# Kernel optimization log

Measured on AMD Instinct MI355X. Metric: run time of the kernel, lower is better.

Reference implementation:

```python
import jax, jax.numpy as jnp
import numpy as np

DIM = 1024
NUM_HEADS = 16
HEAD_DIM = DIM // NUM_HEADS
MLP_RATIO = 4
NUM_EXPERTS = 4
B, N = 4, 1024


def _ln(x, g, b, eps=1e-5):
    m = jnp.mean(x, axis=-1, keepdims=True)
    v = jnp.mean(jnp.square(x - m), axis=-1, keepdims=True)
    return (x - m) * jax.lax.rsqrt(v + eps) * g + b


def setup_inputs() -> dict:
    key = jax.random.key(0)
    ks = jax.random.split(key, 8)
    d = DIM
    return {
        "x": jax.random.normal(ks[0], (B, N, d), jnp.float32),
        "expert_mask": jax.random.randint(ks[1], (B, N), 0, NUM_EXPERTS),
        "expert_probs": jax.random.uniform(ks[2], (B, N, 1), jnp.float32),
        "expand_weight": 0.02 * jax.random.normal(ks[3], (3 * d + MLP_RATIO * d, d), jnp.float32),
        "mlp_bias": 0.02 * jax.random.normal(ks[4], (MLP_RATIO * d,), jnp.float32),
        "contract_weight": 0.02 * jax.random.normal(ks[5], (2 * d, d + MLP_RATIO * d), jnp.float32),
        "contract_bias": 0.02 * jax.random.normal(ks[6], (2 * d,), jnp.float32),
        "norm1_g": jnp.ones((d,), jnp.float32),
        "norm1_b": jnp.zeros((d,), jnp.float32),
        "norm2_g": jnp.ones((d,), jnp.float32),
        "norm2_b": jnp.zeros((d,), jnp.float32),
        "alpha": 0.1 * jax.random.normal(ks[7], (1,), jnp.float32),
    }


def reference(x, expert_mask, expert_probs, expand_weight, mlp_bias, contract_weight,
              contract_bias, norm1_g, norm1_b, norm2_g, norm2_b, alpha):
    Bx, Nx, D = x.shape
    # nested capacity per token: D_e = D // 2**(E-1-e)
    d_e = D // jnp.power(2, NUM_EXPERTS - 1 - expert_mask)          # [B,N] int
    fmask = (jnp.arange(D) < d_e[..., None]).astype(x.dtype)        # [B,N,D]

    residual = x
    # bias as in source: concat([mlp_bias, zeros(3d)]) added to full expand output
    input_bias = jnp.concatenate([mlp_bias, jnp.zeros((3 * D,), x.dtype)], axis=-1)

    # nested_linear_expand: token uses only first D_e input features
    xn = _ln(x, norm1_g, norm1_b) * fmask
    y = jnp.einsum('bnd,ed->bne', xn, expand_weight) + input_bias   # [B,N,7D]

    qkv = y[..., : 3 * D]
    mlp_hidden = y[..., 3 * D:] + mlp_bias                          # [B,N,4D]

    q = qkv[..., :D]
    k = _ln(qkv[..., D:2 * D], norm2_g, norm2_b)
    v = _ln(qkv[..., 2 * D:], norm2_g, norm2_b)

    def heads(t):
        return t.reshape(Bx, Nx, NUM_HEADS, HEAD_DIM).transpose(0, 2, 1, 3)

    scale = HEAD_DIM ** -0.5
    attn = jax.nn.softmax(jnp.einsum('bhqd,bhkd->bhqk', heads(q) * scale, heads(k)), axis=-1)
    attn_out = jnp.einsum('bhqk,bhkd->bhqd', attn, heads(v)).transpose(0, 2, 1, 3).reshape(Bx, Nx, D)

    h = jnp.concatenate([attn_out, jax.nn.gelu(mlp_hidden, approximate=False)], axis=-1)  # [B,N,5D]
    # nested_linear_contract: only first D_e outputs per D-sized half are produced
    out = jnp.einsum('bnf,of->bno', h, contract_weight) + contract_bias                   # [B,N,2D]
    out = out * jnp.concatenate([fmask, fmask], axis=-1)

    attn_branch = out[..., :D] + residual
    return attn_branch + (alpha * expert_probs + 1.0) * out[..., D:]
```

## Files before the change

kernel.cpp:

```cpp
#include <hip/hip_runtime.h>
#include <hip/hip_bf16.h>

typedef __attribute__((ext_vector_type(8))) short bf16x8;
typedef __attribute__((ext_vector_type(4))) short s16x4;
typedef __attribute__((ext_vector_type(4))) float f32x4;

#define DIM    1024
#define TOKENS 4096
#define NHEAD  16
#define HD     64
#define EXP_N  7168
#define CON_N  2048
#define HF     5120

#define WEXP_OFF 0u
#define XN_OFF   14680064u
#define WC_OFF   0u
#define Q_OFF    23068672u
#define K_OFF    31457280u
#define V_OFF    39845888u
#define H_OFF    48234496u
#define PERM_OFF 90177536u
#define DSRT_OFF 90193920u
#define TMAX_OFF 90210304u
#define OUT2_OFF 23068672u

__device__ __forceinline__ short f2bf(float f) {
  union { __hip_bfloat16 h; short s; } u;
  u.h = __float2bfloat16(f);
  return u.s;
}
__device__ __forceinline__ float bf2f(short s) {
  unsigned int u = ((unsigned int)(unsigned short)s) << 16;
  return __builtin_bit_cast(float, u);
}

__device__ __forceinline__ void gload16(const void* g, void* l) {
  __builtin_amdgcn_global_load_lds((const __attribute__((address_space(1))) void*)g,
                                   (__attribute__((address_space(3))) void*)l,
                                   16, 0, 0);
}

__device__ __forceinline__ void block_reduce_2(float& a, float& b) {
  #pragma unroll
  for (int off = 32; off > 0; off >>= 1) {
    a += __shfl_down(a, off);
    b += __shfl_down(b, off);
  }
  __shared__ float red[2][4];
  int wid = threadIdx.x >> 6, lane = threadIdx.x & 63;
  if (lane == 0) { red[0][wid] = a; red[1][wid] = b; }
  __syncthreads();
  a = red[0][0] + red[0][1] + red[0][2] + red[0][3];
  b = red[1][0] + red[1][1] + red[1][2] + red[1][3];
}

__global__ __launch_bounds__(256) void sort_kernel(const int* __restrict__ emask,
                                                   int* __restrict__ perm,
                                                   int* __restrict__ de_sorted,
                                                   int* __restrict__ tile_demax) {
  __shared__ int cnt[4][256];
  __shared__ int boff[4];
  __shared__ int lm[256];
  const int t = threadIdx.x;
  const int lane = t & 63, w = t >> 6;
  int msk[16];
  int lc4[4] = {0, 0, 0, 0};
  #pragma unroll
  for (int j = 0; j < 16; ++j) { msk[j] = emask[t * 16 + j]; lc4[msk[j]]++; }
  #pragma unroll
  for (int b = 0; b < 4; ++b) cnt[b][t] = lc4[b];
  __syncthreads();
  {
    int v0 = cnt[w][lane * 4], v1 = cnt[w][lane * 4 + 1];
    int v2 = cnt[w][lane * 4 + 2], v3 = cnt[w][lane * 4 + 3];
    int s = v0 + v1 + v2 + v3;
    int inc = s;
    #pragma unroll
    for (int off = 1; off < 64; off <<= 1) {
      int n = __shfl_up(inc, off);
      if (lane >= off) inc += n;
    }
    int ex = inc - s;
    cnt[w][lane * 4]     = ex;
    cnt[w][lane * 4 + 1] = ex + v0;
    cnt[w][lane * 4 + 2] = ex + v0 + v1;
    cnt[w][lane * 4 + 3] = ex + v0 + v1 + v2;
    if (lane == 63) boff[w] = inc;
  }
  __syncthreads();
  if (t == 0) {
    int t0 = boff[0], t1 = boff[1], t2 = boff[2];
    boff[0] = 0; boff[1] = t0; boff[2] = t0 + t1; boff[3] = t0 + t1 + t2;
  }
  __syncthreads();
  int c4[4] = {0, 0, 0, 0};
  #pragma unroll
  for (int j = 0; j < 16; ++j) {
    int b = msk[j];
    int pos = boff[b] + cnt[b][t] + c4[b]++;
    perm[pos] = t * 16 + j;
    de_sorted[pos] = DIM >> (3 - b);
  }
  __syncthreads();
  int mx = 0;
  #pragma unroll
  for (int j = 0; j < 16; ++j) mx = max(mx, de_sorted[t * 16 + j]);
  lm[t] = mx;
  __syncthreads();
  if (t < 32) {
    int m2 = 0;
    #pragma unroll
    for (int j = 0; j < 8; ++j) m2 = max(m2, lm[t * 8 + j]);
    tile_demax[t] = m2;
  }
}

__global__ __launch_bounds__(256) void f2bf_kernel(const float* __restrict__ in,
                                                   short* __restrict__ outp, int n4) {
  for (int i = blockIdx.x * blockDim.x + threadIdx.x; i < n4; i += gridDim.x * blockDim.x) {
    f32x4 xv = *(const f32x4*)(&in[(size_t)i * 4]);
    s16x4 o = { f2bf(xv[0]), f2bf(xv[1]), f2bf(xv[2]), f2bf(xv[3]) };
    *(s16x4*)(&outp[(size_t)i * 4]) = o;
  }
}

__global__ __launch_bounds__(256) void ln1_kernel(const float* __restrict__ x,
                                                  const int* __restrict__ emask,
                                                  const float* __restrict__ g,
                                                  const float* __restrict__ bb,
                                                  short* __restrict__ xn) {
  int m = blockIdx.x, t = threadIdx.x;
  const float* row = x + (size_t)m * DIM;
  f32x4 xv = *(const f32x4*)(&row[t * 4]);
  float s  = xv[0] + xv[1] + xv[2] + xv[3];
  float ss = xv[0] * xv[0] + xv[1] * xv[1] + xv[2] * xv[2] + xv[3] * xv[3];
  block_reduce_2(s, ss);
  float mean = s * (1.0f / DIM);
  float var  = ss * (1.0f / DIM) - mean * mean;
  float inv  = rsqrtf(var + 1e-5f);
  int de = DIM >> (3 - emask[m]);
  s16x4 o;
  #pragma unroll
  for (int jj = 0; jj < 4; ++jj) {
    int c = t * 4 + jj;
    float v = (c < de) ? ((xv[jj] - mean) * inv * g[c] + bb[c]) : 0.f;
    o[jj] = f2bf(v);
  }
  *(s16x4*)(&xn[(size_t)m * DIM + t * 4]) = o;
}

#define GBUF 4096

#define STAGE(Asb, Bsb, kk)                                   \
  do {                                                        \
    gload16(Apw + (kk), (Asb) + chw * 512);                   \
    gload16(Bpw + (kk), (Bsb) + chw * 512);                   \
  } while (0)

#define COMPUTE(Asb, Bsb)                                                     \
  do {                                                                        \
    bf16x8 af[4], bfr[2];                                                     \
    _Pragma("unroll")                                                         \
    for (int i = 0; i < 4; ++i)                                               \
      af[i] = *(const bf16x8*)(&(Asb)[(wr * 64 + i * 16 + lc) * 32 + lgs]);   \
    _Pragma("unroll")                                                         \
    for (int j = 0; j < 2; ++j)                                               \
      bfr[j] = *(const bf16x8*)(&(Bsb)[(wc * 32 + j * 16 + lc) * 32 + lgs]);  \
    __builtin_amdgcn_s_setprio(1);                                            \
    _Pragma("unroll")                                                         \
    for (int i = 0; i < 4; ++i)                                               \
      _Pragma("unroll")                                                       \
      for (int j = 0; j < 2; ++j)                                             \
        acc[i][j] = __builtin_amdgcn_mfma_f32_16x16x32_bf16(af[i], bfr[j],    \
                                                            acc[i][j], 0, 0, 0);\
    __builtin_amdgcn_s_setprio(0);                                            \
  } while (0)

#define VMCNT(n) asm volatile("s_waitcnt vmcnt(" #n ")" ::: "memory")

__device__ __forceinline__ void gemm_core_128(const short* __restrict__ A,
                                              const short* __restrict__ B,
                                              int lda, int ldb, int K,
                                              int m0, int n0,
                                              const int* __restrict__ aperm,
                                              short* AS, short* BS,
                                              f32x4 acc[4][2]) {
  const int tid = threadIdx.x;
  const int lane = tid & 63;
  const int wid = tid >> 6;
  const int wr = wid >> 2, wc = wid & 3;
  const int lg = lane >> 4, lc = lane & 15;
  const int lgs = (lg ^ ((lc >> 1) & 3)) * 8;
  const int r4 = lane >> 2;
  const int c8 = ((lane & 3) ^ ((lane >> 3) & 3)) * 8;
  const int chw = wid;
  int ra = m0 + chw * 16 + r4;
  if (aperm) ra = aperm[ra];
  const short* Apw = A + (size_t)ra * lda + c8;
  const short* Bpw = B + (size_t)(n0 + chw * 16 + r4) * ldb + c8;

  const int nt = K >> 5;
  STAGE(AS + 0 * GBUF, BS + 0 * GBUF, 0);
  STAGE(AS + 1 * GBUF, BS + 1 * GBUF, 32);
  STAGE(AS + 2 * GBUF, BS + 2 * GBUF, 64);
  int cur = 0;
  for (int t = 0; t < nt - 2; ++t) {
    short* Ac = AS + cur * GBUF;
    short* Bc = BS + cur * GBUF;
    VMCNT(4);
    __builtin_amdgcn_s_barrier();
    COMPUTE(Ac, Bc);
    __builtin_amdgcn_s_barrier();
    if (t < nt - 3) STAGE(Ac, Bc, (t + 3) * 32);
    cur = (cur == 2) ? 0 : cur + 1;
  }
  {
    short* Ac = AS + cur * GBUF;
    short* Bc = BS + cur * GBUF;
    VMCNT(2);
    __builtin_amdgcn_s_barrier();
    COMPUTE(Ac, Bc);
    cur = (cur == 2) ? 0 : cur + 1;
  }
  {
    short* Ac = AS + cur * GBUF;
    short* Bc = BS + cur * GBUF;
    VMCNT(0);
    __builtin_amdgcn_s_barrier();
    COMPUTE(Ac, Bc);
  }
}

__device__ __forceinline__ void xcd_swizzle_cm(int& bx, int& by) {
  int nwg = gridDim.x * gridDim.y;
  int bid = blockIdx.y * gridDim.x + blockIdx.x;
  int cpx = nwg >> 3;
  int swz = (bid & 7) * cpx + (bid >> 3);
  by = swz % gridDim.y;
  bx = swz / gridDim.y;
}

__global__ __launch_bounds__(512) void gemm1_kernel(const short* __restrict__ xn,
                                                    const short* __restrict__ Wexp,
                                                    const float* __restrict__ mlpb,
                                                    const int* __restrict__ perm,
                                                    const int* __restrict__ tmax,
                                                    short* __restrict__ qbuf,
                                                    short* __restrict__ kbuf,
                                                    short* __restrict__ vbuf,
                                                    short* __restrict__ hbuf) {
  __shared__ __align__(16) short AS[3 * GBUF];
  __shared__ __align__(16) short BS[3 * GBUF];
  f32x4 acc[4][2];
  f32x4 z = {0.f, 0.f, 0.f, 0.f};
  #pragma unroll
  for (int i = 0; i < 4; ++i)
    #pragma unroll
    for (int j = 0; j < 2; ++j) acc[i][j] = z;
  int bx, by;
  xcd_swizzle_cm(bx, by);
  int n0 = bx * 128;
  int m0 = by * 128;
  int kmax = tmax[by];
  gemm_core_128(xn, Wexp, DIM, DIM, kmax, m0, n0, perm, AS, BS, acc);
  const int tid = threadIdx.x, lane = tid & 63, wid = tid >> 6;
  const int wr = wid >> 2, wc = wid & 3, lg = lane >> 4, lc = lane & 15;
  int toks[4][4];
  #pragma unroll
  for (int i = 0; i < 4; ++i)
    #pragma unroll
    for (int r = 0; r < 4; ++r)
      toks[i][r] = perm[m0 + wr * 64 + i * 16 + lg * 4 + r];
  #pragma unroll
  for (int i = 0; i < 4; ++i) {
    #pragma unroll
    for (int j = 0; j < 2; ++j) {
      int e = n0 + wc * 32 + j * 16 + lc;
      #pragma unroll
      for (int r = 0; r < 4; ++r) {
        int m = toks[i][r];
        float val = acc[i][j][r];
        if (e < DIM) {
          qbuf[(size_t)m * DIM + e] = f2bf((val + mlpb[e]) * 0.125f);
        } else if (e < 2 * DIM) {
          kbuf[(size_t)m * DIM + (e - DIM)] = f2bf(val + mlpb[e]);
        } else if (e < 3 * DIM) {
          vbuf[(size_t)m * DIM + (e - 2 * DIM)] = f2bf(val + mlpb[e]);
        } else {
          int jj = e - 3 * DIM;
          float xx = val + mlpb[jj] + (e < 4 * DIM ? mlpb[e] : 0.f);
          float ge = 0.5f * xx * (1.f + erff(xx * 0.70710678118654752f));
          hbuf[(size_t)m * HF + DIM + jj] = f2bf(ge);
        }
      }
    }
  }
}

__global__ __launch_bounds__(256) void ln2_kernel(short* __restrict__ kbuf,
                                                  short* __restrict__ vbuf,
                                                  const float* __restrict__ g,
                                                  const float* __restrict__ bb) {
  int rr = blockIdx.x;
  int m = rr >> 1;
  short* row = ((rr & 1) ? vbuf : kbuf) + (size_t)m * DIM;
  int t = threadIdx.x;
  s16x4 iv = *(const s16x4*)(&row[t * 4]);
  float f[4];
  #pragma unroll
  for (int jj = 0; jj < 4; ++jj) f[jj] = bf2f(iv[jj]);
  float s = f[0] + f[1] + f[2] + f[3];
  float ss = f[0] * f[0] + f[1] * f[1] + f[2] * f[2] + f[3] * f[3];
  block_reduce_2(s, ss);
  float mean = s * (1.0f / DIM);
  float var  = ss * (1.0f / DIM) - mean * mean;
  float inv  = rsqrtf(var + 1e-5f);
  s16x4 o;
  #pragma unroll
  for (int jj = 0; jj < 4; ++jj) {
    int c = t * 4 + jj;
    o[jj] = f2bf((f[jj] - mean) * inv * g[c] + bb[c]);
  }
  *(s16x4*)(&row[t * 4]) = o;
}

__global__ __launch_bounds__(256) void attn_kernel(const short* __restrict__ q,
                                                   const short* __restrict__ k,
                                                   const short* __restrict__ v,
                                                   short* __restrict__ hbuf) {
  __shared__ __align__(16) short Kt[64 * 72];
  __shared__ __align__(16) short Vt[64 * 72];
  __shared__ __align__(16) short Pl[4][16 * 72];
  const int bh = blockIdx.x;
  const int b = bh >> 4, hh = bh & 15;
  const int qt = blockIdx.y;
  const int tid = threadIdx.x, w = tid >> 6, lane = tid & 63;
  const int lg = lane >> 4, lc = lane & 15;

  bf16x8 qa0, qa1;
  {
    const short* qbase = q + ((size_t)(b * 1024 + qt * 64 + w * 16 + lc)) * DIM + hh * HD;
    qa0 = *(const bf16x8*)(qbase + lg * 8);
    qa1 = *(const bf16x8*)(qbase + 32 + lg * 8);
  }
  f32x4 po[4];
  f32x4 z = {0.f, 0.f, 0.f, 0.f};
  #pragma unroll
  for (int d = 0; d < 4; ++d) po[d] = z;
  float mrun[4] = {-INFINITY, -INFINITY, -INFINITY, -INFINITY};
  float lsum[4] = {0.f, 0.f, 0.f, 0.f};

  for (int kt = 0; kt < 16; ++kt) {
    __syncthreads();
    const int kc0 = kt * 64;
    #pragma unroll
    for (int it = 0; it < 2; ++it) {
      int row = (tid >> 3) + it * 32;
      int c8 = (tid & 7) * 8;
      size_t gb = ((size_t)(b * 1024 + kc0 + row)) * DIM + hh * HD + c8;
      *(bf16x8*)(&Kt[row * 72 + c8]) = *(const bf16x8*)(&k[gb]);
      bf16x8 vv = *(const bf16x8*)(&v[gb]);
      #pragma unroll
      for (int jj = 0; jj < 8; ++jj) Vt[(c8 + jj) * 72 + row] = vv[jj];
    }
    __syncthreads();
    f32x4 sacc[4];
    #pragma unroll
    for (int cb = 0; cb < 4; ++cb) {
      bf16x8 kb0 = *(const bf16x8*)(&Kt[(cb * 16 + lc) * 72 + lg * 8]);
      bf16x8 kb1 = *(const bf16x8*)(&Kt[(cb * 16 + lc) * 72 + 32 + lg * 8]);
      f32x4 t0 = __builtin_amdgcn_mfma_f32_16x16x32_bf16(qa0, kb0, z, 0, 0, 0);
      sacc[cb] = __builtin_amdgcn_mfma_f32_16x16x32_bf16(qa1, kb1, t0, 0, 0, 0);
    }
    #pragma unroll
    for (int r = 0; r < 4; ++r) {
      float mx = fmaxf(fmaxf(sacc[0][r], sacc[1][r]), fmaxf(sacc[2][r], sacc[3][r]));
      #pragma unroll
      for (int off = 1; off < 16; off <<= 1) mx = fmaxf(mx, __shfl_xor(mx, off));
      float mnew = fmaxf(mrun[r], mx);
      float al = __expf(mrun[r] - mnew);
      mrun[r] = mnew;
      float ps = 0.f;
      #pragma unroll
      for (int cb = 0; cb < 4; ++cb) {
        float p = __expf(sacc[cb][r] - mnew);
        sacc[cb][r] = p;
        ps += p;
      }
      #pragma unroll
      for (int off = 1; off < 16; off <<= 1) ps += __shfl_xor(ps, off);
      lsum[r] = lsum[r] * al + ps;
      #pragma unroll
      for (int d = 0; d < 4; ++d) po[d][r] *= al;
    }
    #pragma unroll
    for (int cb = 0; cb < 4; ++cb)
      #pragma unroll
      for (int r = 0; r < 4; ++r)
        Pl[w][(lg * 4 + r) * 72 + cb * 16 + lc] = f2bf(sacc[cb][r]);
    __syncthreads();
    bf16x8 pa0 = *(const bf16x8*)(&Pl[w][lc * 72 + lg * 8]);
    bf16x8 pa1 = *(const bf16x8*)(&Pl[w][lc * 72 + 32 + lg * 8]);
    #pragma unroll
    for (int d = 0; d < 4; ++d) {
      bf16x8 vb0 = *(const bf16x8*)(&Vt[(d * 16 + lc) * 72 + lg * 8]);
      bf16x8 vb1 = *(const bf16x8*)(&Vt[(d * 16 + lc) * 72 + 32 + lg * 8]);
      po[d] = __builtin_amdgcn_mfma_f32_16x16x32_bf16(pa0, vb0, po[d], 0, 0, 0);
      po[d] = __builtin_amdgcn_mfma_f32_16x16x32_bf16(pa1, vb1, po[d], 0, 0, 0);
    }
  }
  #pragma unroll
  for (int d = 0; d < 4; ++d)
    #pragma unroll
    for (int r = 0; r < 4; ++r) {
      int token = b * 1024 + qt * 64 + w * 16 + lg * 4 + r;
      float o = po[d][r] / lsum[r];
      hbuf[(size_t)token * HF + hh * HD + d * 16 + lc] = f2bf(o);
    }
}

__global__ __launch_bounds__(512) void gemm2_kernel(const short* __restrict__ h,
                                                    const short* __restrict__ Wc,
                                                    const float* __restrict__ cbias,
                                                    const int* __restrict__ perm,
                                                    const int* __restrict__ dsrt,
                                                    const int* __restrict__ tmax,
                                                    short* __restrict__ out2) {
  __shared__ __align__(16) short AS[3 * GBUF];
  __shared__ __align__(16) short BS[3 * GBUF];
  f32x4 acc[4][2];
  f32x4 z = {0.f, 0.f, 0.f, 0.f};
  #pragma unroll
  for (int i = 0; i < 4; ++i)
    #pragma unroll
    for (int j = 0; j < 2; ++j) acc[i][j] = z;
  int bx, by;
  xcd_swizzle_cm(bx, by);
  int n0 = bx * 128;
  int m0 = by * 128;
  int demax = tmax[by];
  if ((n0 & (DIM - 1)) < demax)
    gemm_core_128(h, Wc, HF, HF, HF, m0, n0, perm, AS, BS, acc);
  const int tid = threadIdx.x, lane = tid & 63, wid = tid >> 6;
  const int wr = wid >> 2, wc = wid & 3, lg = lane >> 4, lc = lane & 15;
  int toks[4][4], des[4][4];
  #pragma unroll
  for (int i = 0; i < 4; ++i)
    #pragma unroll
    for (int r = 0; r < 4; ++r) {
      int ms = m0 + wr * 64 + i * 16 + lg * 4 + r;
      toks[i][r] = perm[ms];
      des[i][r] = dsrt[ms];
    }
  #pragma unroll
  for (int i = 0; i < 4; ++i) {
    #pragma unroll
    for (int j = 0; j < 2; ++j) {
      int o = n0 + wc * 32 + j * 16 + lc;
      float bias = cbias[o];
      #pragma unroll
      for (int r = 0; r < 4; ++r) {
        float val = acc[i][j][r] + bias;
        if ((o & (DIM - 1)) >= des[i][r]) val = 0.f;
        out2[(size_t)toks[i][r] * CON_N + o] = f2bf(val);
      }
    }
  }
}

__global__ __launch_bounds__(256) void combine_kernel(const float* __restrict__ x,
                                                      const float* __restrict__ probs,
                                                      const float* __restrict__ alpha,
                                                      const short* __restrict__ out2,
                                                      float* __restrict__ out) {
  int m = blockIdx.x, t = threadIdx.x;
  float coef = alpha[0] * probs[m] + 1.0f;
  f32x4 xv = *(const f32x4*)(&x[(size_t)m * DIM + t * 4]);
  s16x4 o1 = *(const s16x4*)(&out2[(size_t)m * CON_N + t * 4]);
  s16x4 o2 = *(const s16x4*)(&out2[(size_t)m * CON_N + DIM + t * 4]);
  f32x4 r;
  #pragma unroll
  for (int jj = 0; jj < 4; ++jj) r[jj] = xv[jj] + bf2f(o1[jj]) + coef * bf2f(o2[jj]);
  *(f32x4*)(&out[(size_t)m * DIM + t * 4]) = r;
}

extern "C" void kernel_launch(void* const* d_in, const int* in_sizes, int n_in,
                              void* d_out, int out_size, void* d_ws, size_t ws_size,
                              hipStream_t stream) {
  (void)in_sizes; (void)n_in; (void)out_size; (void)ws_size;
  const float* x     = (const float*)d_in[0];
  const int*   emask = (const int*)d_in[1];
  const float* probs = (const float*)d_in[2];
  const float* Wexp  = (const float*)d_in[3];
  const float* mlpb  = (const float*)d_in[4];
  const float* Wc    = (const float*)d_in[5];
  const float* cbias = (const float*)d_in[6];
  const float* n1g   = (const float*)d_in[7];
  const float* n1b   = (const float*)d_in[8];
  const float* n2g   = (const float*)d_in[9];
  const float* n2b   = (const float*)d_in[10];
  const float* alpha = (const float*)d_in[11];
  float* out = (float*)d_out;
  char* ws = (char*)d_ws;

  short* wexp_bf = (short*)(ws + WEXP_OFF);
  short* xn      = (short*)(ws + XN_OFF);
  short* wc_bf   = (short*)(ws + WC_OFF);
  short* qbuf    = (short*)(ws + Q_OFF);
  short* kbuf    = (short*)(ws + K_OFF);
  short* vbuf    = (short*)(ws + V_OFF);
  short* hbuf    = (short*)(ws + H_OFF);
  short* out2    = (short*)(ws + OUT2_OFF);
  int*   perm    = (int*)(ws + PERM_OFF);
  int*   dsrt    = (int*)(ws + DSRT_OFF);
  int*   tmaxb   = (int*)(ws + TMAX_OFF);

  hipLaunchKernelGGL(sort_kernel, dim3(1), dim3(256), 0, stream, emask, perm, dsrt, tmaxb);
  hipLaunchKernelGGL(f2bf_kernel, dim3(2048), dim3(256), 0, stream, Wexp, wexp_bf, (EXP_N * DIM) / 4);
  hipLaunchKernelGGL(ln1_kernel, dim3(TOKENS), dim3(256), 0, stream, x, emask, n1g, n1b, xn);
  hipLaunchKernelGGL(gemm1_kernel, dim3(EXP_N / 128, TOKENS / 128), dim3(512), 0, stream,
                     xn, wexp_bf, mlpb, perm, tmaxb, qbuf, kbuf, vbuf, hbuf);
  hipLaunchKernelGGL(f2bf_kernel, dim3(2048), dim3(256), 0, stream, Wc, wc_bf, (CON_N * HF) / 4);
  hipLaunchKernelGGL(ln2_kernel, dim3(2 * TOKENS), dim3(256), 0, stream, kbuf, vbuf, n2g, n2b);
  hipLaunchKernelGGL(attn_kernel, dim3(64, 16), dim3(256), 0, stream, qbuf, kbuf, vbuf, hbuf);
  hipLaunchKernelGGL(gemm2_kernel, dim3(CON_N / 128, TOKENS / 128), dim3(512), 0, stream,
                     hbuf, wc_bf, cbias, perm, dsrt, tmaxb, out2);
  hipLaunchKernelGGL(combine_kernel, dim3(TOKENS), dim3(256), 0, stream, x, probs, alpha, out2, out);
}
```

Before: 311.8 us.

## Shrink GEMM M-tile to 64 rows with 4-wave blocks for finer expert skipping

Both GEMMs now use 64x128 tiles with 256-thread blocks instead of 128x128 with 512 threads. Each wave covers all 64 rows and loads two B chunks, and the sort kernel now emits a per-64-token max capacity. The finer M granularity lets more tiles stop early on K in gemm1 or skip entirely in gemm2, and adds blocks for occupancy. In exchange the B operand gets less reuse, so more LDS and global traffic is spent per unit of MFMA work.

```diff
diff --git a/kernel.cpp b/kernel.cpp
--- a/kernel.cpp
+++ b/kernel.cpp
@@ -108,10 +108,10 @@
   for (int j = 0; j < 16; ++j) mx = max(mx, de_sorted[t * 16 + j]);
   lm[t] = mx;
   __syncthreads();
-  if (t < 32) {
+  if (t < 64) {
     int m2 = 0;
     #pragma unroll
-    for (int j = 0; j < 8; ++j) m2 = max(m2, lm[t * 8 + j]);
+    for (int j = 0; j < 4; ++j) m2 = max(m2, lm[t * 4 + j]);
     tile_demax[t] = m2;
   }
 }
@@ -150,12 +150,14 @@
   *(s16x4*)(&xn[(size_t)m * DIM + t * 4]) = o;
 }
 
-#define GBUF 4096
+#define ABUF 2048
+#define BBUF 4096
 
 #define STAGE(Asb, Bsb, kk)                                   \
   do {                                                        \
-    gload16(Apw + (kk), (Asb) + chw * 512);                   \
-    gload16(Bpw + (kk), (Bsb) + chw * 512);                   \
+    gload16(Apw + (kk), (Asb) + wid * 512);                   \
+    gload16(Bpw0 + (kk), (Bsb) + (2 * wid) * 512);            \
+    gload16(Bpw1 + (kk), (Bsb) + (2 * wid + 1) * 512);        \
   } while (0)
 
 #define COMPUTE(Asb, Bsb)                                                     \
@@ -163,10 +165,10 @@
     bf16x8 af[4], bfr[2];                                                     \
     _Pragma("unroll")                                                         \
     for (int i = 0; i < 4; ++i)                                               \
-      af[i] = *(const bf16x8*)(&(Asb)[(wr * 64 + i * 16 + lc) * 32 + lgs]);   \
+      af[i] = *(const bf16x8*)(&(Asb)[(i * 16 + lc) * 32 + lgs]);             \
     _Pragma("unroll")                                                         \
     for (int j = 0; j < 2; ++j)                                               \
-      bfr[j] = *(const bf16x8*)(&(Bsb)[(wc * 32 + j * 16 + lc) * 32 + lgs]);  \
+      bfr[j] = *(const bf16x8*)(&(Bsb)[(wid * 32 + j * 16 + lc) * 32 + lgs]); \
     __builtin_amdgcn_s_setprio(1);                                            \
     _Pragma("unroll")                                                         \
     for (int i = 0; i < 4; ++i)                                               \
@@ -179,36 +181,35 @@
 
 #define VMCNT(n) asm volatile("s_waitcnt vmcnt(" #n ")" ::: "memory")
 
-__device__ __forceinline__ void gemm_core_128(const short* __restrict__ A,
-                                              const short* __restrict__ B,
-                                              int lda, int ldb, int K,
-                                              int m0, int n0,
-                                              const int* __restrict__ aperm,
-                                              short* AS, short* BS,
-                                              f32x4 acc[4][2]) {
+__device__ __forceinline__ void gemm_core_64(const short* __restrict__ A,
+                                             const short* __restrict__ B,
+                                             int lda, int ldb, int K,
+                                             int m0, int n0,
+                                             const int* __restrict__ aperm,
+                                             short* AS, short* BS,
+                                             f32x4 acc[4][2]) {
   const int tid = threadIdx.x;
   const int lane = tid & 63;
   const int wid = tid >> 6;
-  const int wr = wid >> 2, wc = wid & 3;
   const int lg = lane >> 4, lc = lane & 15;
   const int lgs = (lg ^ ((lc >> 1) & 3)) * 8;
   const int r4 = lane >> 2;
   const int c8 = ((lane & 3) ^ ((lane >> 3) & 3)) * 8;
-  const int chw = wid;
-  int ra = m0 + chw * 16 + r4;
+  int ra = m0 + wid * 16 + r4;
   if (aperm) ra = aperm[ra];
-  const short* Apw = A + (size_t)ra * lda + c8;
-  const short* Bpw = B + (size_t)(n0 + chw * 16 + r4) * ldb + c8;
+  const short* Apw  = A + (size_t)ra * lda + c8;
+  const short* Bpw0 = B + (size_t)(n0 + (2 * wid) * 16 + r4) * ldb + c8;
+  const short* Bpw1 = B + (size_t)(n0 + (2 * wid + 1) * 16 + r4) * ldb + c8;
 
   const int nt = K >> 5;
-  STAGE(AS + 0 * GBUF, BS + 0 * GBUF, 0);
-  STAGE(AS + 1 * GBUF, BS + 1 * GBUF, 32);
-  STAGE(AS + 2 * GBUF, BS + 2 * GBUF, 64);
+  STAGE(AS + 0 * ABUF, BS + 0 * BBUF, 0);
+  STAGE(AS + 1 * ABUF, BS + 1 * BBUF, 32);
+  STAGE(AS + 2 * ABUF, BS + 2 * BBUF, 64);
   int cur = 0;
   for (int t = 0; t < nt - 2; ++t) {
-    short* Ac = AS + cur * GBUF;
-    short* Bc = BS + cur * GBUF;
-    VMCNT(4);
+    short* Ac = AS + cur * ABUF;
+    short* Bc = BS + cur * BBUF;
+    VMCNT(6);
     __builtin_amdgcn_s_barrier();
     COMPUTE(Ac, Bc);
     __builtin_amdgcn_s_barrier();
@@ -216,16 +217,16 @@
     cur = (cur == 2) ? 0 : cur + 1;
   }
   {
-    short* Ac = AS + cur * GBUF;
-    short* Bc = BS + cur * GBUF;
-    VMCNT(2);
+    short* Ac = AS + cur * ABUF;
+    short* Bc = BS + cur * BBUF;
+    VMCNT(3);
     __builtin_amdgcn_s_barrier();
     COMPUTE(Ac, Bc);
     cur = (cur == 2) ? 0 : cur + 1;
   }
   {
-    short* Ac = AS + cur * GBUF;
-    short* Bc = BS + cur * GBUF;
+    short* Ac = AS + cur * ABUF;
+    short* Bc = BS + cur * BBUF;
     VMCNT(0);
     __builtin_amdgcn_s_barrier();
     COMPUTE(Ac, Bc);
@@ -241,7 +242,7 @@
   bx = swz / gridDim.y;
 }
 
-__global__ __launch_bounds__(512) void gemm1_kernel(const short* __restrict__ xn,
+__global__ __launch_bounds__(256) void gemm1_kernel(const short* __restrict__ xn,
                                                     const short* __restrict__ Wexp,
                                                     const float* __restrict__ mlpb,
                                                     const int* __restrict__ perm,
@@ -250,8 +251,8 @@
                                                     short* __restrict__ kbuf,
                                                     short* __restrict__ vbuf,
                                                     short* __restrict__ hbuf) {
-  __shared__ __align__(16) short AS[3 * GBUF];
-  __shared__ __align__(16) short BS[3 * GBUF];
+  __shared__ __align__(16) short AS[3 * ABUF];
+  __shared__ __align__(16) short BS[3 * BBUF];
   f32x4 acc[4][2];
   f32x4 z = {0.f, 0.f, 0.f, 0.f};
   #pragma unroll
@@ -261,22 +262,22 @@
   int bx, by;
   xcd_swizzle_cm(bx, by);
   int n0 = bx * 128;
-  int m0 = by * 128;
+  int m0 = by * 64;
   int kmax = tmax[by];
-  gemm_core_128(xn, Wexp, DIM, DIM, kmax, m0, n0, perm, AS, BS, acc);
+  gemm_core_64(xn, Wexp, DIM, DIM, kmax, m0, n0, perm, AS, BS, acc);
   const int tid = threadIdx.x, lane = tid & 63, wid = tid >> 6;
-  const int wr = wid >> 2, wc = wid & 3, lg = lane >> 4, lc = lane & 15;
+  const int lg = lane >> 4, lc = lane & 15;
   int toks[4][4];
   #pragma unroll
   for (int i = 0; i < 4; ++i)
     #pragma unroll
     for (int r = 0; r < 4; ++r)
-      toks[i][r] = perm[m0 + wr * 64 + i * 16 + lg * 4 + r];
+      toks[i][r] = perm[m0 + i * 16 + lg * 4 + r];
   #pragma unroll
   for (int i = 0; i < 4; ++i) {
     #pragma unroll
     for (int j = 0; j < 2; ++j) {
-      int e = n0 + wc * 32 + j * 16 + lc;
+      int e = n0 + wid * 32 + j * 16 + lc;
       #pragma unroll
       for (int r = 0; r < 4; ++r) {
         int m = toks[i][r];
@@ -420,15 +421,15 @@
     }
 }
 
-__global__ __launch_bounds__(512) void gemm2_kernel(const short* __restrict__ h,
+__global__ __launch_bounds__(256) void gemm2_kernel(const short* __restrict__ h,
                                                     const short* __restrict__ Wc,
                                                     const float* __restrict__ cbias,
                                                     const int* __restrict__ perm,
                                                     const int* __restrict__ dsrt,
                                                     const int* __restrict__ tmax,
                                                     short* __restrict__ out2) {
-  __shared__ __align__(16) short AS[3 * GBUF];
-  __shared__ __align__(16) short BS[3 * GBUF];
+  __shared__ __align__(16) short AS[3 * ABUF];
+  __shared__ __align__(16) short BS[3 * BBUF];
   f32x4 acc[4][2];
   f32x4 z = {0.f, 0.f, 0.f, 0.f};
   #pragma unroll
@@ -438,18 +439,18 @@
   int bx, by;
   xcd_swizzle_cm(bx, by);
   int n0 = bx * 128;
-  int m0 = by * 128;
+  int m0 = by * 64;
   int demax = tmax[by];
   if ((n0 & (DIM - 1)) < demax)
-    gemm_core_128(h, Wc, HF, HF, HF, m0, n0, perm, AS, BS, acc);
+    gemm_core_64(h, Wc, HF, HF, HF, m0, n0, perm, AS, BS, acc);
   const int tid = threadIdx.x, lane = tid & 63, wid = tid >> 6;
-  const int wr = wid >> 2, wc = wid & 3, lg = lane >> 4, lc = lane & 15;
+  const int lg = lane >> 4, lc = lane & 15;
   int toks[4][4], des[4][4];
   #pragma unroll
   for (int i = 0; i < 4; ++i)
     #pragma unroll
     for (int r = 0; r < 4; ++r) {
-      int ms = m0 + wr * 64 + i * 16 + lg * 4 + r;
+      int ms = m0 + i * 16 + lg * 4 + r;
       toks[i][r] = perm[ms];
       des[i][r] = dsrt[ms];
     }
@@ -457,7 +458,7 @@
   for (int i = 0; i < 4; ++i) {
     #pragma unroll
     for (int j = 0; j < 2; ++j) {
-      int o = n0 + wc * 32 + j * 16 + lc;
+      int o = n0 + wid * 32 + j * 16 + lc;
       float bias = cbias[o];
       #pragma unroll
       for (int r = 0; r < 4; ++r) {
@@ -519,12 +520,12 @@
   hipLaunchKernelGGL(sort_kernel, dim3(1), dim3(256), 0, stream, emask, perm, dsrt, tmaxb);
   hipLaunchKernelGGL(f2bf_kernel, dim3(2048), dim3(256), 0, stream, Wexp, wexp_bf, (EXP_N * DIM) / 4);
   hipLaunchKernelGGL(ln1_kernel, dim3(TOKENS), dim3(256), 0, stream, x, emask, n1g, n1b, xn);
-  hipLaunchKernelGGL(gemm1_kernel, dim3(EXP_N / 128, TOKENS / 128), dim3(512), 0, stream,
+  hipLaunchKernelGGL(gemm1_kernel, dim3(EXP_N / 128, TOKENS / 64), dim3(256), 0, stream,
                      xn, wexp_bf, mlpb, perm, tmaxb, qbuf, kbuf, vbuf, hbuf);
   hipLaunchKernelGGL(f2bf_kernel, dim3(2048), dim3(256), 0, stream, Wc, wc_bf, (CON_N * HF) / 4);
   hipLaunchKernelGGL(ln2_kernel, dim3(2 * TOKENS), dim3(256), 0, stream, kbuf, vbuf, n2g, n2b);
   hipLaunchKernelGGL(attn_kernel, dim3(64, 16), dim3(256), 0, stream, qbuf, kbuf, vbuf, hbuf);
-  hipLaunchKernelGGL(gemm2_kernel, dim3(CON_N / 128, TOKENS / 128), dim3(512), 0, stream,
+  hipLaunchKernelGGL(gemm2_kernel, dim3(CON_N / 128, TOKENS / 64), dim3(256), 0, stream,
                      hbuf, wc_bf, cbias, perm, dsrt, tmaxb, out2);
   hipLaunchKernelGGL(combine_kernel, dim3(TOKENS), dim3(256), 0, stream, x, probs, alpha, out2, out);
 }
```

New measurement: 373.2 us. 19.7% more time.

## Pre-transpose V in a separate kernel and drop a barrier in attention

Applied to the files above, without the earlier changes.

Adds a kernel that transposes V into a head-dim-major buffer once, so the attention kernel loads V tiles with 16-byte vector stores into LDS instead of eight scalar transposed stores per thread on every key tile. It also removes a block-wide barrier before reading each wave's private P tile, which only that wave writes. The cost is one extra launch and an extra 8 MB read/write pass over V. Dropping the barrier relies on same-wave LDS write/read ordering within a wave.

```diff
diff --git a/kernel.cpp b/kernel.cpp
--- a/kernel.cpp
+++ b/kernel.cpp
@@ -23,6 +23,7 @@
 #define PERM_OFF 90177536u
 #define DSRT_OFF 90193920u
 #define TMAX_OFF 90210304u
+#define VT_OFF   90210560u
 #define OUT2_OFF 23068672u
 
 __device__ __forceinline__ short f2bf(float f) {
@@ -325,9 +326,33 @@
   *(s16x4*)(&row[t * 4]) = o;
 }
 
+__global__ __launch_bounds__(256) void vtrans_kernel(const short* __restrict__ v,
+                                                     short* __restrict__ vt) {
+  __shared__ short tl[64][72];
+  const int bidx = blockIdx.x;
+  const int kt = bidx & 15, dt = (bidx >> 4) & 15, b = bidx >> 8;
+  const int tid = threadIdx.x;
+  const int row = tid >> 3, c8 = (tid & 7) * 8;
+  #pragma unroll
+  for (int it = 0; it < 2; ++it) {
+    int r = row + it * 32;
+    *(bf16x8*)(&tl[r][c8]) =
+      *(const bf16x8*)(&v[((size_t)(b * 1024 + kt * 64 + r)) * DIM + dt * 64 + c8]);
+  }
+  __syncthreads();
+  #pragma unroll
+  for (int it = 0; it < 2; ++it) {
+    int d = row + it * 32;
+    bf16x8 o;
+    #pragma unroll
+    for (int jj = 0; jj < 8; ++jj) o[jj] = tl[c8 + jj][d];
+    *(bf16x8*)(&vt[((size_t)(b * 1024 + dt * 64 + d)) * 1024 + kt * 64 + c8]) = o;
+  }
+}
+
 __global__ __launch_bounds__(256) void attn_kernel(const short* __restrict__ q,
                                                    const short* __restrict__ k,
-                                                   const short* __restrict__ v,
+                                                   const short* __restrict__ vt,
                                                    short* __restrict__ hbuf) {
   __shared__ __align__(16) short Kt[64 * 72];
   __shared__ __align__(16) short Vt[64 * 72];
@@ -358,11 +383,10 @@
     for (int it = 0; it < 2; ++it) {
       int row = (tid >> 3) + it * 32;
       int c8 = (tid & 7) * 8;
-      size_t gb = ((size_t)(b * 1024 + kc0 + row)) * DIM + hh * HD + c8;
-      *(bf16x8*)(&Kt[row * 72 + c8]) = *(const bf16x8*)(&k[gb]);
-      bf16x8 vv = *(const bf16x8*)(&v[gb]);
-      #pragma unroll
-      for (int jj = 0; jj < 8; ++jj) Vt[(c8 + jj) * 72 + row] = vv[jj];
+      size_t gk = ((size_t)(b * 1024 + kc0 + row)) * DIM + hh * HD + c8;
+      *(bf16x8*)(&Kt[row * 72 + c8]) = *(const bf16x8*)(&k[gk]);
+      size_t gv = ((size_t)(b * 1024 + hh * HD + row)) * 1024 + kc0 + c8;
+      *(bf16x8*)(&Vt[row * 72 + c8]) = *(const bf16x8*)(&vt[gv]);
     }
     __syncthreads();
     f32x4 sacc[4];
@@ -399,7 +423,6 @@
       #pragma unroll
       for (int r = 0; r < 4; ++r)
         Pl[w][(lg * 4 + r) * 72 + cb * 16 + lc] = f2bf(sacc[cb][r]);
-    __syncthreads();
     bf16x8 pa0 = *(const bf16x8*)(&Pl[w][lc * 72 + lg * 8]);
     bf16x8 pa1 = *(const bf16x8*)(&Pl[w][lc * 72 + 32 + lg * 8]);
     #pragma unroll
@@ -511,6 +534,7 @@
   short* kbuf    = (short*)(ws + K_OFF);
   short* vbuf    = (short*)(ws + V_OFF);
   short* hbuf    = (short*)(ws + H_OFF);
+  short* vtbuf   = (short*)(ws + VT_OFF);
   short* out2    = (short*)(ws + OUT2_OFF);
   int*   perm    = (int*)(ws + PERM_OFF);
   int*   dsrt    = (int*)(ws + DSRT_OFF);
@@ -523,7 +547,8 @@
                      xn, wexp_bf, mlpb, perm, tmaxb, qbuf, kbuf, vbuf, hbuf);
   hipLaunchKernelGGL(f2bf_kernel, dim3(2048), dim3(256), 0, stream, Wc, wc_bf, (CON_N * HF) / 4);
   hipLaunchKernelGGL(ln2_kernel, dim3(2 * TOKENS), dim3(256), 0, stream, kbuf, vbuf, n2g, n2b);
-  hipLaunchKernelGGL(attn_kernel, dim3(64, 16), dim3(256), 0, stream, qbuf, kbuf, vbuf, hbuf);
+  hipLaunchKernelGGL(vtrans_kernel, dim3(1024), dim3(256), 0, stream, vbuf, vtbuf);
+  hipLaunchKernelGGL(attn_kernel, dim3(64, 16), dim3(256), 0, stream, qbuf, kbuf, vtbuf, hbuf);
   hipLaunchKernelGGL(gemm2_kernel, dim3(CON_N / 128, TOKENS / 128), dim3(512), 0, stream,
                      hbuf, wc_bf, cbias, perm, dsrt, tmaxb, out2);
   hipLaunchKernelGGL(combine_kernel, dim3(TOKENS), dim3(256), 0, stream, x, probs, alpha, out2, out);
```

New measurement: 288.5 us, median of 2. 1.08x faster.
